# Kernel optimization log

Measured on AMD Instinct MI355X. Metric: run time of the kernel, lower is better.

The kernel has to match this reference:

```python
import jax, jax.numpy as jnp
import numpy as np

HIDDEN = 1024
N_HEAD = 16
LN_EPS = 1e-5


def _layernorm(x, g, b):
    m = jnp.mean(x, axis=-1, keepdims=True)
    v = jnp.var(x, axis=-1, keepdims=True)
    return (x - m) * jax.lax.rsqrt(v + LN_EPS) * g + b


def setup_inputs() -> dict:
    key = jax.random.key(0)
    ks = jax.random.split(key, 16)
    H = HIDDEN
    s = 0.02
    d = dict(
        x=jax.random.normal(ks[0], (4, 1024, H), jnp.float32),
        Wq=jax.random.normal(ks[1], (H, H), jnp.float32) * s,
        bq=jnp.zeros((H,), jnp.float32),
        Wk=jax.random.normal(ks[2], (H, H), jnp.float32) * s,
        bk=jnp.zeros((H,), jnp.float32),
        Wv=jax.random.normal(ks[3], (H, H), jnp.float32) * s,
        bv=jnp.zeros((H,), jnp.float32),
        Wo=jax.random.normal(ks[4], (H, H), jnp.float32) * s,
        bo=jnp.zeros((H,), jnp.float32),
        g1=jax.random.normal(ks[5], (H,), jnp.float32) * s,
        b1=jnp.zeros((H,), jnp.float32),
        W1=jax.random.normal(ks[6], (H, 4 * H), jnp.float32) * s,
        c1=jnp.zeros((4 * H,), jnp.float32),
        W2=jax.random.normal(ks[7], (4 * H, H), jnp.float32) * s,
        c2=jnp.zeros((H,), jnp.float32),
        g2=jax.random.normal(ks[8], (H,), jnp.float32) * s,
        b2=jnp.zeros((H,), jnp.float32),
    )
    return d


def reference(x, Wq, bq, Wk, bk, Wv, bv, Wo, bo, g1, b1, W1, c1, W2, c2, g2, b2):
    N, T, Hd = x.shape
    Hh = N_HEAD
    D = Hd // Hh
    # faithful to torch code: .view(N, H, T, D) is a raw reshape, no transpose
    q = (x @ Wq + bq).reshape(N, Hh, T, D)
    k = (x @ Wk + bk).reshape(N, Hh, T, D)
    v = (x @ Wv + bv).reshape(N, Hh, T, D)
    scores = jnp.einsum('nhtd,nhsd->nhts', q, k) / jnp.sqrt(jnp.float32(Hd))
    # faithful: softmax over dim=1 (the head axis)
    attn = jax.nn.softmax(scores, axis=1)
    o = jnp.einsum('nhts,nhsd->nhtd', attn, v).reshape(N, T, Hd)
    o = o @ Wo + bo
    x1 = _layernorm(o + x, g1, b1)
    ff = jax.nn.gelu(x1 @ W1 + c1, approximate=False) @ W2 + c2
    return _layernorm(ff + x1, g2, b2)
```

## Files before the change

### kernel.cpp

```cpp
#include <hip/hip_runtime.h>
#include <cstdint>
#include <cstddef>

#define EPI_QKV  0
#define EPI_F32  2
#define EPI_GELU 3
#define EPI_PART 4

typedef __attribute__((ext_vector_type(8))) short bfrag8;
typedef __attribute__((ext_vector_type(4))) float facc4;

struct PtrQuad { unsigned short* p[4]; };

__device__ __forceinline__ unsigned short f2b(float x) {
  unsigned int u = __builtin_bit_cast(unsigned int, x);
  u += 0x7FFFu + ((u >> 16) & 1u);
  return (unsigned short)(u >> 16);
}
__device__ __forceinline__ float b2f(unsigned short u) {
  unsigned int x = ((unsigned int)u) << 16;
  return __builtin_bit_cast(float, x);
}

__device__ __forceinline__ void gl2lds16(const unsigned short* g, unsigned short* l) {
  __builtin_amdgcn_global_load_lds(
      (const __attribute__((address_space(1))) unsigned int*)g,
      (__attribute__((address_space(3))) unsigned int*)l, 16, 0, 0);
}

__global__ __launch_bounds__(256)
void cvt_bf16_kernel(const float* __restrict__ in, unsigned short* __restrict__ out, int n4) {
  const int i = blockIdx.x * 256 + threadIdx.x;
  if (i < n4) {
    const float4 v = ((const float4*)in)[i];
    ushort4 u;
    u.x = f2b(v.x); u.y = f2b(v.y); u.z = f2b(v.z); u.w = f2b(v.w);
    ((ushort4*)out)[i] = u;
  }
}

__global__ __launch_bounds__(256)
void transpose_cvt(const float* __restrict__ in, unsigned short* __restrict__ out,
                   int K, int N) {
  __shared__ float tile[32][33];
  const int n0 = blockIdx.x * 32;
  const int k0 = blockIdx.y * 32;
  const int tx = threadIdx.x & 31, ty = threadIdx.x >> 5;
#pragma unroll
  for (int i = 0; i < 32; i += 8)
    tile[ty + i][tx] = in[(size_t)(k0 + ty + i) * N + n0 + tx];
  __syncthreads();
#pragma unroll
  for (int i = 0; i < 32; i += 8)
    out[(size_t)(n0 + ty + i) * K + k0 + tx] = f2b(tile[tx][ty + i]);
}

template<int EPI>
__global__ __launch_bounds__(256, 2)
void gemm_bt(const unsigned short* __restrict__ A,
             const unsigned short* __restrict__ Bt,
             const float* __restrict__ bias,
             const float* __restrict__ bias2,
             const float* __restrict__ bias3,
             void* __restrict__ out, PtrQuad pq,
             int M, int N, int K, int ldk) {
  __shared__ unsigned short sA[128 * 32];
  __shared__ unsigned short sB[128 * 32];
  const int tid  = threadIdx.x;
  const int lane = tid & 63;
  const int wave = tid >> 6;
  const int l15  = lane & 15, l4 = lane >> 4;
  const int wr = wave >> 1, wc = wave & 1;
  const long row0 = (long)blockIdx.y * 128;
  const long col0 = (long)blockIdx.x * 128;
  const long k0   = (long)blockIdx.z * K;

  facc4 acc[4][4];
#pragma unroll
  for (int i = 0; i < 4; i++)
#pragma unroll
    for (int j = 0; j < 4; j++) acc[i][j] = (facc4)0.f;

  const int srow = tid >> 2;
  const int scol = (tid & 3) * 8;
  const unsigned short* Ap0 = A  + (row0 + srow) * (long)ldk + k0 + scol;
  const unsigned short* Ap1 = Ap0 + 64 * (long)ldk;
  const unsigned short* Bp0 = Bt + (col0 + srow) * (long)ldk + k0 + scol;
  const unsigned short* Bp1 = Bp0 + 64 * (long)ldk;
  const int wbase = (tid & ~63) * 8;
  unsigned short* sA0 = &sA[wbase];
  unsigned short* sA1 = &sA[2048 + wbase];
  unsigned short* sB0 = &sB[wbase];
  unsigned short* sB1 = &sB[2048 + wbase];

  const int aoff = (wr * 64 + l15) * 32 + l4 * 8;
  const int boff = (wc * 64 + l15) * 32 + l4 * 8;

  for (int kt = 0; kt < K; kt += 32) {
    gl2lds16(Ap0 + kt, sA0);
    gl2lds16(Ap1 + kt, sA1);
    gl2lds16(Bp0 + kt, sB0);
    gl2lds16(Bp1 + kt, sB1);
    __syncthreads();
    bfrag8 af[4], bf[4];
#pragma unroll
    for (int i = 0; i < 4; i++) af[i] = *(const bfrag8*)&sA[aoff + i * 512];
#pragma unroll
    for (int j = 0; j < 4; j++) bf[j] = *(const bfrag8*)&sB[boff + j * 512];
#pragma unroll
    for (int i = 0; i < 4; i++)
#pragma unroll
      for (int j = 0; j < 4; j++)
        acc[i][j] = __builtin_amdgcn_mfma_f32_16x16x32_bf16(af[i], bf[j], acc[i][j], 0, 0, 0);
    __syncthreads();
  }

#pragma unroll
  for (int i = 0; i < 4; i++) {
    const long m0 = row0 + wr * 64 + i * 16 + l4 * 4;
#pragma unroll
    for (int j = 0; j < 4; j++) {
      const long c = col0 + wc * 64 + j * 16 + l15;
      if constexpr (EPI == EPI_QKV) {
        const long which = c >> 10;
        const long cl = c & 1023;
        unsigned short* oq = (unsigned short*)out;
        if (which == 0) {
          const float bj = bias[cl];
#pragma unroll
          for (int r = 0; r < 4; r++)
            oq[(m0 + r) * 1024 + cl] = f2b((acc[i][j][r] + bj) * 0.03125f);
        } else if (which == 1) {
          const float bj = bias2[cl];
#pragma unroll
          for (int r = 0; r < 4; r++)
            (oq + 4194304)[(m0 + r) * 1024 + cl] = f2b(acc[i][j][r] + bj);
        } else {
          const float bj = bias3[cl];
          const long cc = cl >> 6, d = cl & 63;
#pragma unroll
          for (int r = 0; r < 4; r++) {
            const long m = m0 + r;
            const long nbb = m >> 10, rr = m & 1023;
            const long h = rr >> 6, rhi = rr & 63;
            const long s = rhi * 16 + cc;
            (oq + 8388608)[((nbb * 16 + h) * 64 + d) * 1024 + s] = f2b(acc[i][j][r] + bj);
          }
        }
      } else if constexpr (EPI == EPI_F32) {
        const float bj = bias[c];
        float* of = (float*)out;
#pragma unroll
        for (int r = 0; r < 4; r++) of[(m0 + r) * (long)N + c] = acc[i][j][r] + bj;
      } else if constexpr (EPI == EPI_PART) {
        unsigned short* ob = pq.p[blockIdx.z];
#pragma unroll
        for (int r = 0; r < 4; r++) ob[(m0 + r) * (long)N + c] = f2b(acc[i][j][r]);
      } else {
        const float bj = bias[c];
        unsigned short* ob = (unsigned short*)out;
#pragma unroll
        for (int r = 0; r < 4; r++) {
          const float t = acc[i][j][r] + bj;
          ob[(m0 + r) * (long)N + c] = f2b(0.5f * t * (1.f + erff(t * 0.70710678f)));
        }
      }
    }
  }
}

__global__ __launch_bounds__(512, 1)
void attn_kernel(const unsigned short* __restrict__ Qb,
                 const unsigned short* __restrict__ Kb,
                 const unsigned short* __restrict__ Vt,
                 unsigned short* __restrict__ P0, unsigned short* __restrict__ P1) {
  const int id = blockIdx.x;
  const int combo = id & 7;
  const int nb = combo & 3;
  const int sp = combo >> 2;
  const int tile = id >> 3;
  const int tid = threadIdx.x, lane = tid & 63;
  const int w = __builtin_amdgcn_readfirstlane(tid >> 6);
  const int l15 = lane & 15, l4 = lane >> 4;
  const int t0 = tile * 32;
  const int sbase = sp * 512;
  const int h0 = w * 2;

  __shared__ __align__(16) unsigned short Qs[16 * 32 * 64];
  __shared__ float Ds[8][64][33];
  __shared__ __align__(16) unsigned short Pw[8][1024];

  const size_t bb = ((size_t)(nb * 16)) << 16;
  const unsigned short* qB = Qb + bb;
  const unsigned short* kB = Kb + bb;
  const unsigned short* vB = Vt + bb;

#pragma unroll
  for (int kk = 0; kk < 8; kk++) {
    const int j = kk * 512 + tid;
    const int h = j >> 8, t = (j >> 3) & 31, d8 = j & 7;
    const int4 v = *(const int4*)(qB + ((size_t)h << 16) + (size_t)(t0 + t) * 64 + d8 * 8);
    *(int4*)((char*)Qs + h * 4096 + t * 128 + ((d8 * 16) ^ ((t & 7) << 4))) = v;
  }

  const int swz = (l15 & 7) << 4;
  char* pw = (char*)&Pw[w][0];
  const int pwrow = l15 * 128;

  facc4 oacc[2][2][4];
#pragma unroll
  for (int hh = 0; hh < 2; hh++)
#pragma unroll
    for (int ts = 0; ts < 2; ts++)
#pragma unroll
      for (int nt = 0; nt < 4; nt++) oacc[hh][ts][nt] = (facc4)0.f;

  __syncthreads();

  for (int it = 0; it < 8; ++it) {
    const int s0 = sbase + it * 64;
    bfrag8 kf[2][4][2];
#pragma unroll
    for (int hh = 0; hh < 2; hh++) {
      const unsigned short* kh_ = kB + ((size_t)(h0 + hh) << 16) + (size_t)l15 * 64 + l4 * 8;
#pragma unroll
      for (int ss = 0; ss < 4; ss++)
#pragma unroll
        for (int kh = 0; kh < 2; kh++)
          kf[hh][ss][kh] = *(const bfrag8*)(kh_ + (size_t)(s0 + ss * 16) * 64 + kh * 32);
    }
    bfrag8 vf[2][2][4];
#pragma unroll
    for (int hh = 0; hh < 2; hh++) {
      const unsigned short* vh_ = vB + ((size_t)(h0 + hh) << 16) + (size_t)l15 * 1024 + s0 + l4 * 8;
#pragma unroll
      for (int sk = 0; sk < 2; sk++)
#pragma unroll
        for (int nt = 0; nt < 4; nt++)
          vf[hh][sk][nt] = *(const bfrag8*)(vh_ + (size_t)(nt * 16) * 1024 + sk * 32);
    }
    facc4 sc[2][2][4];
#pragma unroll
    for (int hh = 0; hh < 2; hh++)
#pragma unroll
      for (int ts = 0; ts < 2; ts++) {
        const char* qh = (const char*)Qs + (h0 + hh) * 4096 + (ts * 16 + l15) * 128;
        const bfrag8 q0 = *(const bfrag8*)(qh + ((l4 * 16) ^ swz));
        const bfrag8 q1 = *(const bfrag8*)(qh + ((64 + l4 * 16) ^ swz));
#pragma unroll
        for (int ss = 0; ss < 4; ss++) {
          facc4 a = __builtin_amdgcn_mfma_f32_16x16x32_bf16(kf[hh][ss][0], q0, (facc4)0.f, 0, 0, 0);
          sc[hh][ts][ss] = __builtin_amdgcn_mfma_f32_16x16x32_bf16(kf[hh][ss][1], q1, a, 0, 0, 0);
        }
      }
    facc4 dacc[2][4];
#pragma unroll
    for (int ts = 0; ts < 2; ts++)
#pragma unroll
      for (int ss = 0; ss < 4; ss++) dacc[ts][ss] = (facc4)0.f;
#pragma unroll
    for (int hh = 0; hh < 2; hh++)
#pragma unroll
      for (int ts = 0; ts < 2; ts++)
#pragma unroll
        for (int ss = 0; ss < 4; ss++)
#pragma unroll
          for (int r = 0; r < 4; r++) {
            const float e = __expf(sc[hh][ts][ss][r]);
            sc[hh][ts][ss][r] = e;
            dacc[ts][ss][r] += e;
          }
#pragma unroll
    for (int ts = 0; ts < 2; ts++)
#pragma unroll
      for (int ss = 0; ss < 4; ss++)
#pragma unroll
        for (int r = 0; r < 4; r++)
          Ds[w][ss * 16 + l4 * 4 + r][ts * 16 + l15] = dacc[ts][ss][r];
    __syncthreads();
    facc4 rt[2][4];
#pragma unroll
    for (int ts = 0; ts < 2; ts++)
#pragma unroll
      for (int ss = 0; ss < 4; ss++)
#pragma unroll
        for (int r = 0; r < 4; r++) {
          const int si = ss * 16 + l4 * 4 + r;
          const int ti = ts * 16 + l15;
          float s_ = Ds[0][si][ti];
#pragma unroll
          for (int ww = 1; ww < 8; ww++) s_ += Ds[ww][si][ti];
          rt[ts][ss][r] = 1.f / s_;
        }
#pragma unroll
    for (int hh = 0; hh < 2; hh++)
#pragma unroll
      for (int ts = 0; ts < 2; ts++) {
#pragma unroll
        for (int ss = 0; ss < 4; ss++) {
          const float p0 = sc[hh][ts][ss][0] * rt[ts][ss][0];
          const float p1 = sc[hh][ts][ss][1] * rt[ts][ss][1];
          const float p2 = sc[hh][ts][ss][2] * rt[ts][ss][2];
          const float p3 = sc[hh][ts][ss][3] * rt[ts][ss][3];
          uint2 pk;
          asm("v_cvt_pk_bf16_f32 %0, %1, %2" : "=v"(pk.x) : "v"(p0), "v"(p1));
          asm("v_cvt_pk_bf16_f32 %0, %1, %2" : "=v"(pk.y) : "v"(p2), "v"(p3));
          *(uint2*)(pw + pwrow + ((ss * 32 + l4 * 8) ^ swz)) = pk;
        }
        const bfrag8 a0 = *(const bfrag8*)(pw + pwrow + ((l4 * 16) ^ swz));
        const bfrag8 a1 = *(const bfrag8*)(pw + pwrow + ((64 + l4 * 16) ^ swz));
#pragma unroll
        for (int nt = 0; nt < 4; nt++) {
          oacc[hh][ts][nt] = __builtin_amdgcn_mfma_f32_16x16x32_bf16(a0, vf[hh][0][nt],
                                                                    oacc[hh][ts][nt], 0, 0, 0);
          oacc[hh][ts][nt] = __builtin_amdgcn_mfma_f32_16x16x32_bf16(a1, vf[hh][1][nt],
                                                                    oacc[hh][ts][nt], 0, 0, 0);
        }
      }
    __syncthreads();
  }

  unsigned short* P = sp ? P1 : P0;
#pragma unroll
  for (int hh = 0; hh < 2; hh++) {
    const size_t hb = ((size_t)nb << 20) + ((size_t)(h0 + hh) << 16);
#pragma unroll
    for (int ts = 0; ts < 2; ts++)
#pragma unroll
      for (int nt = 0; nt < 4; nt++)
#pragma unroll
        for (int r = 0; r < 4; r++)
          P[hb + (size_t)(t0 + ts * 16 + l4 * 4 + r) * 64 + nt * 16 + l15] =
              f2b(oacc[hh][ts][nt][r]);
  }
}

__global__ __launch_bounds__(256)
void reduce_o2(const unsigned short* __restrict__ P0, const unsigned short* __restrict__ P1,
               unsigned short* __restrict__ OB, int n4) {
  const int i = blockIdx.x * 256 + threadIdx.x;
  if (i < n4) {
    const ushort4 a = ((const ushort4*)P0)[i];
    const ushort4 b = ((const ushort4*)P1)[i];
    ushort4 u;
    u.x = f2b(b2f(a.x) + b2f(b.x));
    u.y = f2b(b2f(a.y) + b2f(b.y));
    u.z = f2b(b2f(a.z) + b2f(b.z));
    u.w = f2b(b2f(a.w) + b2f(b.w));
    ((ushort4*)OB)[i] = u;
  }
}

__global__ __launch_bounds__(256)
void ln_red(const unsigned short* __restrict__ P0, const unsigned short* __restrict__ P1,
            const unsigned short* __restrict__ P2, const unsigned short* __restrict__ P3,
            const float* __restrict__ bias, const float* __restrict__ resid,
            const float* __restrict__ g, const float* __restrict__ be,
            float* __restrict__ outf, unsigned short* __restrict__ outb) {
  const int row = blockIdx.x, tid = threadIdx.x;
  const size_t o4 = (size_t)row * 256 + tid;
  const ushort4 a = ((const ushort4*)P0)[o4];
  const ushort4 b = ((const ushort4*)P1)[o4];
  const ushort4 c = ((const ushort4*)P2)[o4];
  const ushort4 d = ((const ushort4*)P3)[o4];
  const float4 vb = ((const float4*)bias)[tid];
  const float4 vr = ((const float4*)resid)[o4];
  float t0 = b2f(a.x) + b2f(b.x) + b2f(c.x) + b2f(d.x) + vb.x + vr.x;
  float t1 = b2f(a.y) + b2f(b.y) + b2f(c.y) + b2f(d.y) + vb.y + vr.y;
  float t2 = b2f(a.z) + b2f(b.z) + b2f(c.z) + b2f(d.z) + vb.z + vr.z;
  float t3 = b2f(a.w) + b2f(b.w) + b2f(c.w) + b2f(d.w) + vb.w + vr.w;
  float s = t0 + t1 + t2 + t3;
  float q = t0 * t0 + t1 * t1 + t2 * t2 + t3 * t3;
#pragma unroll
  for (int off = 32; off > 0; off >>= 1) {
    s += __shfl_down(s, off, 64);
    q += __shfl_down(q, off, 64);
  }
  __shared__ float rs_[4], rq_[4];
  if ((tid & 63) == 0) { rs_[tid >> 6] = s; rq_[tid >> 6] = q; }
  __syncthreads();
  const float S = rs_[0] + rs_[1] + rs_[2] + rs_[3];
  const float Q = rq_[0] + rq_[1] + rq_[2] + rq_[3];
  const float mean = S * (1.f / 1024.f);
  const float var  = Q * (1.f / 1024.f) - mean * mean;
  const float rstd = rsqrtf(var + 1e-5f);
  const float4 vg  = ((const float4*)g)[tid];
  const float4 vbe = ((const float4*)be)[tid];
  float o0 = (t0 - mean) * rstd * vg.x + vbe.x;
  float o1 = (t1 - mean) * rstd * vg.y + vbe.y;
  float o2 = (t2 - mean) * rstd * vg.z + vbe.z;
  float o3 = (t3 - mean) * rstd * vg.w + vbe.w;
  ((float4*)(outf + (size_t)row * 1024))[tid] = make_float4(o0, o1, o2, o3);
  if (outb != nullptr) {
    ushort4 u;
    u.x = f2b(o0); u.y = f2b(o1); u.z = f2b(o2); u.w = f2b(o3);
    ((ushort4*)(outb + (size_t)row * 1024))[tid] = u;
  }
}

extern "C" void kernel_launch(void* const* d_in, const int* in_sizes, int n_in,
                              void* d_out, int out_size, void* d_ws, size_t ws_size,
                              hipStream_t stream) {
  const float* x  = (const float*)d_in[0];
  const float* Wq = (const float*)d_in[1];
  const float* bq = (const float*)d_in[2];
  const float* Wk = (const float*)d_in[3];
  const float* bk = (const float*)d_in[4];
  const float* Wv = (const float*)d_in[5];
  const float* bv = (const float*)d_in[6];
  const float* Wo = (const float*)d_in[7];
  const float* bo = (const float*)d_in[8];
  const float* g1 = (const float*)d_in[9];
  const float* b1 = (const float*)d_in[10];
  const float* W1 = (const float*)d_in[11];
  const float* c1 = (const float*)d_in[12];
  const float* W2 = (const float*)d_in[13];
  const float* c2 = (const float*)d_in[14];
  const float* g2 = (const float*)d_in[15];
  const float* b2 = (const float*)d_in[16];
  float* out = (float*)d_out;

  char* ws = (char*)d_ws;
  unsigned short* XB  = (unsigned short*)(ws);
  unsigned short* WQT = (unsigned short*)(ws + 8388608);
  unsigned short* WKT = (unsigned short*)(ws + 10485760);
  unsigned short* WVT = (unsigned short*)(ws + 12582912);
  unsigned short* WOT = (unsigned short*)(ws + 14680064);
  unsigned short* W1T = (unsigned short*)(ws + 16777216);
  unsigned short* W2T = (unsigned short*)(ws + 25165824);
  float*          X1  = (float*)(ws + 33554432);
  unsigned short* X1B = (unsigned short*)(ws + 50331648);
  char* RB = ws + 58720256;
  unsigned short* QB  = (unsigned short*)(RB);
  unsigned short* KB  = (unsigned short*)(RB + 8388608);
  unsigned short* VT  = (unsigned short*)(RB + 16777216);
  unsigned short* OB  = (unsigned short*)(RB + 25165824);
  unsigned short* H1B = (unsigned short*)(RB);
  unsigned short* AP0 = (unsigned short*)(RB + 33554432);
  unsigned short* AP1 = (unsigned short*)(RB + 41943040);
  PtrQuad OPQ = { { QB, KB, VT, XB } };
  PtrQuad FPQ = { { XB, X1B, (unsigned short*)(RB + 33554432),
                    (unsigned short*)(RB + 41943040) } };
  PtrQuad ZQ = { { nullptr, nullptr, nullptr, nullptr } };

  const dim3 tb(256);
  cvt_bf16_kernel<<<dim3(4096), tb, 0, stream>>>(x, XB, 1048576);
  transpose_cvt<<<dim3(32, 32),  tb, 0, stream>>>(Wq, WQT, 1024, 1024);
  transpose_cvt<<<dim3(32, 32),  tb, 0, stream>>>(Wk, WKT, 1024, 1024);
  transpose_cvt<<<dim3(32, 32),  tb, 0, stream>>>(Wv, WVT, 1024, 1024);
  transpose_cvt<<<dim3(32, 32),  tb, 0, stream>>>(Wo, WOT, 1024, 1024);
  transpose_cvt<<<dim3(128, 32), tb, 0, stream>>>(W1, W1T, 1024, 4096);
  transpose_cvt<<<dim3(32, 128), tb, 0, stream>>>(W2, W2T, 4096, 1024);
  gemm_bt<EPI_QKV><<<dim3(24, 32), tb, 0, stream>>>(XB, WQT, bq, bk, bv, (void*)QB, ZQ,
                                                    4096, 3072, 1024, 1024);
  attn_kernel<<<dim3(256), dim3(512), 0, stream>>>(QB, KB, VT, AP0, AP1);
  reduce_o2<<<dim3(4096), tb, 0, stream>>>(AP0, AP1, OB, 1048576);
  gemm_bt<EPI_PART><<<dim3(8, 32, 4), tb, 0, stream>>>(OB, WOT, nullptr, nullptr, nullptr,
                                                       nullptr, OPQ, 4096, 1024, 256, 1024);
  ln_red<<<dim3(4096), tb, 0, stream>>>(QB, KB, VT, XB, bo, x, g1, b1, X1, X1B);
  gemm_bt<EPI_GELU><<<dim3(32, 32), tb, 0, stream>>>(X1B, W1T, c1, nullptr, nullptr,
                                                     (void*)H1B, ZQ, 4096, 4096, 1024, 1024);
  gemm_bt<EPI_PART><<<dim3(8, 32, 4), tb, 0, stream>>>(H1B, W2T, nullptr, nullptr, nullptr,
                                                       nullptr, FPQ, 4096, 1024, 1024, 4096);
  ln_red<<<dim3(4096), tb, 0, stream>>>(FPQ.p[0], FPQ.p[1], FPQ.p[2], FPQ.p[3], c2, X1,
                                        g2, b2, out, (unsigned short*)nullptr);
}
```

Before: 448.3 us.

## Keep Q in registers and cooperatively reduce cross-head softmax denominators

Q fragments are now loaded straight from global memory into registers, so the Q staging buffer in LDS and its barrier are gone. The per-wave partial denominators are stored transposed as float4 vectors. Each thread then sums one float4 across the 8 waves into a shared Dt table, replacing the old scheme where every thread redundantly summed 32 values across 8 waves. The reciprocal uses the hardware rcp, the score MFMAs are issued before the V loads, and the trailing per-iteration barrier is dropped in exchange for one added barrier in the reduction.

```diff
diff --git a/kernel.cpp b/kernel.cpp
--- a/kernel.cpp
+++ b/kernel.cpp
@@ -186,8 +186,8 @@
   const int sbase = sp * 512;
   const int h0 = w * 2;
 
-  __shared__ __align__(16) unsigned short Qs[16 * 32 * 64];
-  __shared__ float Ds[8][64][33];
+  __shared__ __align__(16) float Ds[8][32][68];
+  __shared__ __align__(16) float Dt[32][68];
   __shared__ __align__(16) unsigned short Pw[8][1024];
 
   const size_t bb = ((size_t)(nb * 16)) << 16;
@@ -195,17 +195,21 @@
   const unsigned short* kB = Kb + bb;
   const unsigned short* vB = Vt + bb;
 
-#pragma unroll
-  for (int kk = 0; kk < 8; kk++) {
-    const int j = kk * 512 + tid;
-    const int h = j >> 8, t = (j >> 3) & 31, d8 = j & 7;
-    const int4 v = *(const int4*)(qB + ((size_t)h << 16) + (size_t)(t0 + t) * 64 + d8 * 8);
-    *(int4*)((char*)Qs + h * 4096 + t * 128 + ((d8 * 16) ^ ((t & 7) << 4))) = v;
-  }
+  bfrag8 qf[2][2][2];
+#pragma unroll
+  for (int hh = 0; hh < 2; hh++)
+#pragma unroll
+    for (int ts = 0; ts < 2; ts++)
+#pragma unroll
+      for (int dh = 0; dh < 2; dh++)
+        qf[hh][ts][dh] = *(const bfrag8*)(qB + ((size_t)(h0 + hh) << 16)
+            + (size_t)(t0 + ts * 16 + l15) * 64 + dh * 32 + l4 * 8);
 
   const int swz = (l15 & 7) << 4;
   char* pw = (char*)&Pw[w][0];
   const int pwrow = l15 * 128;
+  const int ti1 = tid >> 4;
+  const int si1 = (tid & 15) * 4;
 
   facc4 oacc[2][2][4];
 #pragma unroll
@@ -214,8 +218,6 @@
     for (int ts = 0; ts < 2; ts++)
 #pragma unroll
       for (int nt = 0; nt < 4; nt++) oacc[hh][ts][nt] = (facc4)0.f;
-
-  __syncthreads();
 
   for (int it = 0; it < 8; ++it) {
     const int s0 = sbase + it * 64;
@@ -229,6 +231,18 @@
         for (int kh = 0; kh < 2; kh++)
           kf[hh][ss][kh] = *(const bfrag8*)(kh_ + (size_t)(s0 + ss * 16) * 64 + kh * 32);
     }
+    facc4 sc[2][2][4];
+#pragma unroll
+    for (int hh = 0; hh < 2; hh++)
+#pragma unroll
+      for (int ts = 0; ts < 2; ts++)
+#pragma unroll
+        for (int ss = 0; ss < 4; ss++) {
+          facc4 a = __builtin_amdgcn_mfma_f32_16x16x32_bf16(kf[hh][ss][0], qf[hh][ts][0],
+                                                            (facc4)0.f, 0, 0, 0);
+          sc[hh][ts][ss] = __builtin_amdgcn_mfma_f32_16x16x32_bf16(kf[hh][ss][1],
+                                                                   qf[hh][ts][1], a, 0, 0, 0);
+        }
     bfrag8 vf[2][2][4];
 #pragma unroll
     for (int hh = 0; hh < 2; hh++) {
@@ -239,20 +253,6 @@
         for (int nt = 0; nt < 4; nt++)
           vf[hh][sk][nt] = *(const bfrag8*)(vh_ + (size_t)(nt * 16) * 1024 + sk * 32);
     }
-    facc4 sc[2][2][4];
-#pragma unroll
-    for (int hh = 0; hh < 2; hh++)
-#pragma unroll
-      for (int ts = 0; ts < 2; ts++) {
-        const char* qh = (const char*)Qs + (h0 + hh) * 4096 + (ts * 16 + l15) * 128;
-        const bfrag8 q0 = *(const bfrag8*)(qh + ((l4 * 16) ^ swz));
-        const bfrag8 q1 = *(const bfrag8*)(qh + ((64 + l4 * 16) ^ swz));
-#pragma unroll
-        for (int ss = 0; ss < 4; ss++) {
-          facc4 a = __builtin_amdgcn_mfma_f32_16x16x32_bf16(kf[hh][ss][0], q0, (facc4)0.f, 0, 0, 0);
-          sc[hh][ts][ss] = __builtin_amdgcn_mfma_f32_16x16x32_bf16(kf[hh][ss][1], q1, a, 0, 0, 0);
-        }
-      }
     facc4 dacc[2][4];
 #pragma unroll
     for (int ts = 0; ts < 2; ts++)
@@ -274,24 +274,24 @@
     for (int ts = 0; ts < 2; ts++)
 #pragma unroll
       for (int ss = 0; ss < 4; ss++)
-#pragma unroll
-        for (int r = 0; r < 4; r++)
-          Ds[w][ss * 16 + l4 * 4 + r][ts * 16 + l15] = dacc[ts][ss][r];
+        *(facc4*)&Ds[w][ts * 16 + l15][ss * 16 + l4 * 4] = dacc[ts][ss];
+    __syncthreads();
+    {
+      facc4 s_ = *(const facc4*)&Ds[0][ti1][si1];
+#pragma unroll
+      for (int ww = 1; ww < 8; ww++) s_ += *(const facc4*)&Ds[ww][ti1][si1];
+      *(facc4*)&Dt[ti1][si1] = s_;
+    }
     __syncthreads();
     facc4 rt[2][4];
 #pragma unroll
     for (int ts = 0; ts < 2; ts++)
 #pragma unroll
-      for (int ss = 0; ss < 4; ss++)
-#pragma unroll
-        for (int r = 0; r < 4; r++) {
-          const int si = ss * 16 + l4 * 4 + r;
-          const int ti = ts * 16 + l15;
-          float s_ = Ds[0][si][ti];
-#pragma unroll
-          for (int ww = 1; ww < 8; ww++) s_ += Ds[ww][si][ti];
-          rt[ts][ss][r] = 1.f / s_;
-        }
+      for (int ss = 0; ss < 4; ss++) {
+        const facc4 d = *(const facc4*)&Dt[ts * 16 + l15][ss * 16 + l4 * 4];
+#pragma unroll
+        for (int r = 0; r < 4; r++) rt[ts][ss][r] = __builtin_amdgcn_rcpf(d[r]);
+      }
 #pragma unroll
     for (int hh = 0; hh < 2; hh++)
 #pragma unroll
@@ -317,7 +317,6 @@
                                                                     oacc[hh][ts][nt], 0, 0, 0);
         }
       }
-    __syncthreads();
   }
 
   unsigned short* P = sp ? P1 : P0;
```

Result: faster. 428.8 us (-4.4%).
